# Optimization experiments

Measured on AMD Instinct MI355X. Metric: run time of the kernel, lower is better.

## Reference

```python
import jax, jax.numpy as jnp
import numpy as np

B, T, C, H = 4, 2048, 768, 64

def setup_inputs() -> dict:
    key = jax.random.key(0)
    kx, kq, kk, kv = jax.random.split(key, 4)
    x = jax.random.normal(kx, (B, T, C), dtype=jnp.float32)
    # torch Linear(C->H, bias=False): y = x @ W with W [C, H]
    s = 1.0 / np.sqrt(C)
    Wq = jax.random.normal(kq, (C, H), dtype=jnp.float32) * s
    Wk = jax.random.normal(kk, (C, H), dtype=jnp.float32) * s
    Wv = jax.random.normal(kv, (C, H), dtype=jnp.float32) * s
    return {"x": x, "Wq": Wq, "Wk": Wk, "Wv": Wv}

def reference(x, Wq, Wk, Wv):
    Bx, Tx, Cx = x.shape
    q = jnp.einsum('btc,ch->bth', x, Wq)
    k = jnp.einsum('btc,ch->bth', x, Wk)
    v = jnp.einsum('btc,ch->bth', x, Wv)
    # NOTE: original scales by C**-0.5 (n_embeddings), not head_size**-0.5
    w = jnp.einsum('bqh,bkh->bqk', q, k) * (Cx ** -0.5)  # [B, T, T]
    causal = jnp.tril(jnp.ones((Tx, Tx), dtype=bool))
    w = jnp.where(causal, w, -jnp.inf)
    w = jax.nn.softmax(w, axis=-1)
    # dropout: eval mode (identity)
    out = jnp.einsum('bqk,bkh->bqh', w, v)  # [B, T, H]
    return out
```

## Files before the change

kernel.cpp:

```cpp
#include <hip/hip_runtime.h>
#include <math.h>

#define TB 2048
#define CB 768
#define NB 4
#define NROWS (NB * TB)
#define NSMAX 32
#define WGPB 528

typedef __attribute__((ext_vector_type(8))) short bf16x8;
typedef __attribute__((ext_vector_type(4))) float f32x4;
typedef __attribute__((ext_vector_type(2))) float f32x2;
typedef __attribute__((ext_vector_type(2))) unsigned int u32x2;
typedef __attribute__((ext_vector_type(4))) unsigned int u32x4;

__device__ inline unsigned short f2bf(float f) {
  union { float f; unsigned u; } v; v.f = f;
  unsigned r = v.u + 0x7FFFu + ((v.u >> 16) & 1u);
  return (unsigned short)(r >> 16);
}
__device__ inline unsigned pack2bf(float a, float b) {
  return (unsigned)f2bf(a) | ((unsigned)f2bf(b) << 16);
}
__device__ inline float bf2f(unsigned short u) {
  union { unsigned u; float f; } v; v.u = (unsigned)u << 16; return v.f;
}

__global__ void cvt_w_kernel(const float* __restrict__ Wq, const float* __restrict__ Wk,
                             const float* __restrict__ Wv, unsigned short* __restrict__ Wt) {
  __shared__ float tw[64][65];
  const float* W = (blockIdx.y == 0) ? Wq : (blockIdx.y == 1) ? Wk : Wv;
  const int c0 = blockIdx.x * 64;
  const int row = threadIdx.x >> 2, seg = threadIdx.x & 3;
#pragma unroll
  for (int i = 0; i < 4; ++i) {
    float4 f = *(const float4*)(W + (size_t)(c0 + row) * 64 + seg * 16 + i * 4);
    tw[row][seg * 16 + i * 4 + 0] = f.x;
    tw[row][seg * 16 + i * 4 + 1] = f.y;
    tw[row][seg * 16 + i * 4 + 2] = f.z;
    tw[row][seg * 16 + i * 4 + 3] = f.w;
  }
  __syncthreads();
  const int j = threadIdx.x >> 2, cq = threadIdx.x & 3;
  unsigned short* dst = Wt + (size_t)(blockIdx.y * 64 + j) * CB + c0 + cq * 16;
  u32x4 ua, ub;
#pragma unroll
  for (int i = 0; i < 4; ++i) ua[i] = pack2bf(tw[cq * 16 + 2 * i][j], tw[cq * 16 + 2 * i + 1][j]);
#pragma unroll
  for (int i = 0; i < 4; ++i) ub[i] = pack2bf(tw[cq * 16 + 8 + 2 * i][j], tw[cq * 16 + 9 + 2 * i][j]);
  *(u32x4*)dst = ua;
  *(u32x4*)(dst + 8) = ub;
}

__launch_bounds__(256)
__global__ void proj_direct_kernel(const float* __restrict__ x,
                                   const unsigned short* __restrict__ Wt,
                                   unsigned short* __restrict__ q,
                                   unsigned short* __restrict__ k,
                                   unsigned short* __restrict__ vT) {
  __shared__ __align__(16) unsigned short xs[16 * 64];
  __shared__ float tr[64][17];
  const int tid = threadIdx.x;
  const int wv = tid >> 6;
  const int l = tid & 63;
  const int lrow = l & 15, lg = l >> 4;
  const int m0 = blockIdx.x * 16;
  const int srow = tid >> 4;
  const int sq = tid & 15;
  const float* xp = x + (size_t)(m0 + srow) * CB + sq * 4;
  const int swz = (srow & 7) << 4;

  f32x4 acc[3];
#pragma unroll
  for (int n = 0; n < 3; ++n) acc[n] = (f32x4){0.f, 0.f, 0.f, 0.f};

  float4 f = *(const float4*)xp;
  for (int k0 = 0; k0 < CB; k0 += 64) {
    {
      u32x2 c;
      c.x = pack2bf(f.x, f.y);
      c.y = pack2bf(f.z, f.w);
      *(u32x2*)((char*)xs + srow * 128 + ((sq * 8) ^ swz)) = c;
    }
    if (k0 + 64 < CB) f = *(const float4*)(xp + k0 + 64);
    __syncthreads();

#pragma unroll
    for (int s = 0; s < 2; ++s) {
      bf16x8 af = *(const bf16x8*)((const char*)xs + lrow * 128 +
                                   ((s * 64 + lg * 16) ^ ((lrow & 7) << 4)));
#pragma unroll
      for (int nf = 0; nf < 3; ++nf) {
        int col = wv * 48 + nf * 16 + lrow;
        bf16x8 bfr = *(const bf16x8*)(Wt + (size_t)col * CB + k0 + s * 32 + lg * 8);
        acc[nf] = __builtin_amdgcn_mfma_f32_16x16x32_bf16(af, bfr, acc[nf], 0, 0, 0);
      }
    }
    __syncthreads();
  }

#pragma unroll
  for (int nf = 0; nf < 3; ++nf) {
    int j = wv * 48 + nf * 16 + lrow;
#pragma unroll
    for (int r = 0; r < 4; ++r) {
      int grow = m0 + lg * 4 + r;
      if (j < 64)       q[(size_t)grow * 64 + j] = f2bf(acc[nf][r]);
      else if (j < 128) k[(size_t)grow * 64 + (j - 64)] = f2bf(acc[nf][r]);
      else              tr[j - 128][lg * 4 + r] = acc[nf][r];
    }
  }
  __syncthreads();
  {
    const int b = m0 >> 11, t0 = m0 & (TB - 1);
    const int h = tid >> 2, tq = tid & 3;
    u32x2 pk;
    pk.x = pack2bf(tr[h][tq * 4 + 0], tr[h][tq * 4 + 1]);
    pk.y = pack2bf(tr[h][tq * 4 + 2], tr[h][tq * 4 + 3]);
    *(u32x2*)(vT + ((size_t)(b * 64 + h)) * TB + t0 + tq * 4) = pk;
  }
}

__launch_bounds__(256)
__global__ void attn_kernel(const unsigned short* __restrict__ q,
                            const unsigned short* __restrict__ k,
                            const unsigned short* __restrict__ vT,
                            unsigned short* __restrict__ PO, float* __restrict__ Mp,
                            float* __restrict__ Lp) {
  __shared__ __align__(16) char ksm[8192];
  __shared__ __align__(16) char vsm[8192];
  const int tid = threadIdx.x;
  const int wid = tid >> 6, l = tid & 63;
  const int lrow = l & 15, lg = l >> 4;
  const int b = blockIdx.y;
  const int w = blockIdx.x;

  int g = (int)((sqrtf((float)(8 * w + 1)) - 1.f) * 0.5f);
  while ((g + 1) * (g + 2) / 2 <= w) ++g;
  while (g * (g + 1) / 2 > w) --g;
  const int blk = w - g * (g + 1) / 2;
  const int kv0 = blk * 64;
  const bool last = (blk == g);
  const int qrow = (4 * g + wid) * 16 + lrow;

  const unsigned short* qb = q + (size_t)b * TB * 64;
  const char* kbb = (const char*)(k + (size_t)b * TB * 64);
  const unsigned short* vb = vT + (size_t)b * 64 * TB;

  const int srow = tid >> 2;
  const int sc = (tid & 3) * 32;
  float4 kg0 = *(const float4*)(kbb + (size_t)kv0 * 128 + tid * 32);
  float4 kg1 = *(const float4*)(kbb + (size_t)kv0 * 128 + tid * 32 + 16);
  const char* vrow = (const char*)(vb + (size_t)srow * TB + kv0);
  float4 vg0 = *(const float4*)(vrow + sc);
  float4 vg1 = *(const float4*)(vrow + sc + 16);

  bf16x8 qf[2];
#pragma unroll
  for (int s = 0; s < 2; ++s)
    qf[s] = *(const bf16x8*)(qb + (size_t)qrow * 64 + s * 32 + lg * 8);

  {
    const int kswz_w = (srow & 7) << 4;
    *(float4*)(ksm + srow * 128 + ((sc + 0) ^ kswz_w)) = kg0;
    *(float4*)(ksm + srow * 128 + ((sc + 16) ^ kswz_w)) = kg1;
    const int vswz_w = (srow & 3) << 5;
    *(float4*)(vsm + srow * 128 + ((sc + 0) ^ vswz_w)) = vg0;
    *(float4*)(vsm + srow * 128 + ((sc + 16) ^ vswz_w)) = vg1;
  }
  __syncthreads();

  const int kswz = (lrow & 7) << 4;
  f32x4 S[4];
#pragma unroll
  for (int cf = 0; cf < 4; ++cf) S[cf] = (f32x4){0.f, 0.f, 0.f, 0.f};
#pragma unroll
  for (int cf = 0; cf < 4; ++cf) {
    const char* kp = ksm + (cf * 16 + lrow) * 128;
#pragma unroll
    for (int s = 0; s < 2; ++s) {
      bf16x8 kf = *(const bf16x8*)(kp + ((s * 64 + lg * 16) ^ kswz));
      S[cf] = __builtin_amdgcn_mfma_f32_16x16x32_bf16(kf, qf[s], S[cf], 0, 0, 0);
    }
  }

  const float scale = 0.03608439182435161f;
  float tmx = -INFINITY;
#pragma unroll
  for (int cf = 0; cf < 4; ++cf)
#pragma unroll
    for (int r = 0; r < 4; ++r) {
      float vv = S[cf][r] * scale;
      if (last) {
        int kvi = kv0 + cf * 16 + lg * 4 + r;
        vv = (kvi > qrow) ? -INFINITY : vv;
      }
      S[cf][r] = vv;
      tmx = fmaxf(tmx, vv);
    }
  tmx = fmaxf(tmx, __shfl_xor(tmx, 16));
  tmx = fmaxf(tmx, __shfl_xor(tmx, 32));

  float lsl = 0.f;
  float p[4][4];
#pragma unroll
  for (int cf = 0; cf < 4; ++cf)
#pragma unroll
    for (int r = 0; r < 4; ++r) {
      float pe = __expf(S[cf][r] - tmx);
      p[cf][r] = pe;
      lsl += pe;
    }
  union { unsigned u[4]; bf16x8 v; } pbu[2];
#pragma unroll
  for (int s = 0; s < 2; ++s) {
    pbu[s].u[0] = pack2bf(p[2 * s][0], p[2 * s][1]);
    pbu[s].u[1] = pack2bf(p[2 * s][2], p[2 * s][3]);
    pbu[s].u[2] = pack2bf(p[2 * s + 1][0], p[2 * s + 1][1]);
    pbu[s].u[3] = pack2bf(p[2 * s + 1][2], p[2 * s + 1][3]);
  }

  f32x4 o[4];
#pragma unroll
  for (int hf = 0; hf < 4; ++hf) o[hf] = (f32x4){0.f, 0.f, 0.f, 0.f};
  const int rswz = (lrow & 3) << 5;
#pragma unroll
  for (int s = 0; s < 2; ++s)
#pragma unroll
    for (int hf = 0; hf < 4; ++hf) {
      int r = hf * 16 + lrow;
      int a1 = r * 128 + ((s * 64 + lg * 8) ^ rswz);
      u32x2 lo = *(const u32x2*)(vsm + a1);
      u32x2 hi = *(const u32x2*)(vsm + (a1 ^ 32));
      union { unsigned u[4]; bf16x8 v; } vfu;
      vfu.u[0] = lo.x; vfu.u[1] = lo.y; vfu.u[2] = hi.x; vfu.u[3] = hi.y;
      o[hf] = __builtin_amdgcn_mfma_f32_16x16x32_bf16(vfu.v, pbu[s].v, o[hf], 0, 0, 0);
    }

  float ls = lsl;
  ls += __shfl_xor(ls, 16);
  ls += __shfl_xor(ls, 32);

  size_t rowg = (size_t)blk * NROWS + b * TB + qrow;
  unsigned short* pop = PO + rowg * 64 + lg * 4;
#pragma unroll
  for (int hf = 0; hf < 4; ++hf) {
    u32x2 pk;
    pk.x = pack2bf(o[hf][0], o[hf][1]);
    pk.y = pack2bf(o[hf][2], o[hf][3]);
    *(u32x2*)(pop + hf * 16) = pk;
  }
  if (lg == 0) {
    Mp[rowg] = tmx;
    Lp[rowg] = ls;
  }
}

__global__ void attn_reduce_kernel(const unsigned short* __restrict__ PO,
                                   const float* __restrict__ Mp,
                                   const float* __restrict__ Lp,
                                   float* __restrict__ out) {
  int id = blockIdx.x * 256 + threadIdx.x;
  if (id >= NROWS * 32) return;
  int row = id >> 5, h0 = (id & 31) * 2;
  int t = row & (TB - 1);
  int ns = (t >> 6) + 1;
  float M = -INFINITY;
#pragma unroll 4
  for (int s = 0; s < ns; ++s) M = fmaxf(M, Mp[(size_t)s * NROWS + row]);
  float L = 0.f, a0 = 0.f, a1 = 0.f;
#pragma unroll 4
  for (int s = 0; s < ns; ++s) {
    float w = __expf(Mp[(size_t)s * NROWS + row] - M);
    L += Lp[(size_t)s * NROWS + row] * w;
    unsigned pv = *(const unsigned*)(PO + ((size_t)s * NROWS + row) * 64 + h0);
    a0 += bf2f((unsigned short)(pv & 0xffff)) * w;
    a1 += bf2f((unsigned short)(pv >> 16)) * w;
  }
  float rL = 1.f / L;
  f32x2 r; r.x = a0 * rL; r.y = a1 * rL;
  *(f32x2*)(out + (size_t)row * 64 + h0) = r;
}

extern "C" void kernel_launch(void* const* d_in, const int* in_sizes, int n_in,
                              void* d_out, int out_size, void* d_ws, size_t ws_size,
                              hipStream_t stream) {
  const float* x  = (const float*)d_in[0];
  const float* Wq = (const float*)d_in[1];
  const float* Wk = (const float*)d_in[2];
  const float* Wv = (const float*)d_in[3];
  float* out = (float*)d_out;

  unsigned short* Wt = (unsigned short*)d_ws;
  unsigned short* qb = Wt + 192 * CB;
  unsigned short* kb = qb + (size_t)NROWS * 64;
  unsigned short* vT = kb + (size_t)NROWS * 64;
  char* scratch = (char*)(vT + (size_t)NROWS * 64);

  unsigned short* PO = (unsigned short*)scratch;
  float* Mp = (float*)(scratch + (size_t)NSMAX * NROWS * 64 * 2);
  float* Lp = Mp + (size_t)NSMAX * NROWS;

  hipLaunchKernelGGL(cvt_w_kernel, dim3(12, 3), dim3(256), 0, stream,
                     Wq, Wk, Wv, Wt);
  hipLaunchKernelGGL(proj_direct_kernel, dim3(NROWS / 16), dim3(256), 0, stream,
                     x, Wt, qb, kb, vT);
  hipLaunchKernelGGL(attn_kernel, dim3(WGPB, NB), dim3(256), 0, stream,
                     qb, kb, vT, PO, Mp, Lp);
  hipLaunchKernelGGL(attn_reduce_kernel, dim3((NROWS * 32) / 256), dim3(256), 0, stream,
                     PO, Mp, Lp, out);
}
```

Baseline: 56.76 us.

## Process two 64-key blocks per attention workgroup to halve split partials

Each attention workgroup now loads two consecutive 64-wide K/V blocks (128 keys) into double LDS buffers and computes a joint softmax over both before writing one partial. The number of split partials per query row drops from up to 32 to up to 16, which halves partial-output writes and the reduce kernel's loop and memory traffic. The price is fewer, larger workgroups with more LDS per block, which lowers parallelism and occupancy. The group-index decoding is rewritten for the new per-group block counts.

New measurement: 51.07 us. 10.0% less time.

```diff
diff --git a/kernel.cpp b/kernel.cpp
--- a/kernel.cpp
+++ b/kernel.cpp
@@ -5,8 +5,8 @@
 #define CB 768
 #define NB 4
 #define NROWS (NB * TB)
-#define NSMAX 32
-#define WGPB 528
+#define NSMAX 16
+#define WGPB 272
 
 typedef __attribute__((ext_vector_type(8))) short bf16x8;
 typedef __attribute__((ext_vector_type(4))) float f32x4;
@@ -24,6 +24,10 @@
 }
 __device__ inline float bf2f(unsigned short u) {
   union { unsigned u; float f; } v; v.u = (unsigned)u << 16; return v.f;
+}
+__device__ inline int groupP(int g) {
+  int m = g >> 1;
+  return (g & 1) ? (m + 1) * (m + 1) : m * (m + 1);
 }
 
 __global__ void cvt_w_kernel(const float* __restrict__ Wq, const float* __restrict__ Wk,
@@ -127,20 +131,22 @@
                             const unsigned short* __restrict__ vT,
                             unsigned short* __restrict__ PO, float* __restrict__ Mp,
                             float* __restrict__ Lp) {
-  __shared__ __align__(16) char ksm[8192];
-  __shared__ __align__(16) char vsm[8192];
+  __shared__ __align__(16) char ksm[2][8192];
+  __shared__ __align__(16) char vsm[2][8192];
   const int tid = threadIdx.x;
   const int wid = tid >> 6, l = tid & 63;
   const int lrow = l & 15, lg = l >> 4;
   const int b = blockIdx.y;
   const int w = blockIdx.x;
 
-  int g = (int)((sqrtf((float)(8 * w + 1)) - 1.f) * 0.5f);
-  while ((g + 1) * (g + 2) / 2 <= w) ++g;
-  while (g * (g + 1) / 2 > w) --g;
-  const int blk = w - g * (g + 1) / 2;
-  const int kv0 = blk * 64;
-  const bool last = (blk == g);
+  int g = (int)(2.f * sqrtf((float)w));
+  if (g > 31) g = 31;
+  while (g < 31 && groupP(g + 1) <= w) ++g;
+  while (g > 0 && groupP(g) > w) --g;
+  const int b128 = w - groupP(g);
+  const int s64a = 2 * b128, s64b = 2 * b128 + 1;
+  const bool has1 = (s64b <= g);
+  const int kv0a = s64a * 64, kv0b = s64b * 64;
   const int qrow = (4 * g + wid) * 16 + lrow;
 
   const unsigned short* qb = q + (size_t)b * TB * 64;
@@ -149,99 +155,173 @@
 
   const int srow = tid >> 2;
   const int sc = (tid & 3) * 32;
-  float4 kg0 = *(const float4*)(kbb + (size_t)kv0 * 128 + tid * 32);
-  float4 kg1 = *(const float4*)(kbb + (size_t)kv0 * 128 + tid * 32 + 16);
-  const char* vrow = (const char*)(vb + (size_t)srow * TB + kv0);
-  float4 vg0 = *(const float4*)(vrow + sc);
-  float4 vg1 = *(const float4*)(vrow + sc + 16);
+  const int kswz_w = (srow & 7) << 4;
+  const int vswz_w = (srow & 3) << 5;
+
+  float4 ka0 = *(const float4*)(kbb + (size_t)kv0a * 128 + tid * 32);
+  float4 ka1 = *(const float4*)(kbb + (size_t)kv0a * 128 + tid * 32 + 16);
+  const char* vrowa = (const char*)(vb + (size_t)srow * TB + kv0a);
+  float4 va0 = *(const float4*)(vrowa + sc);
+  float4 va1 = *(const float4*)(vrowa + sc + 16);
 
   bf16x8 qf[2];
 #pragma unroll
   for (int s = 0; s < 2; ++s)
     qf[s] = *(const bf16x8*)(qb + (size_t)qrow * 64 + s * 32 + lg * 8);
 
-  {
-    const int kswz_w = (srow & 7) << 4;
-    *(float4*)(ksm + srow * 128 + ((sc + 0) ^ kswz_w)) = kg0;
-    *(float4*)(ksm + srow * 128 + ((sc + 16) ^ kswz_w)) = kg1;
-    const int vswz_w = (srow & 3) << 5;
-    *(float4*)(vsm + srow * 128 + ((sc + 0) ^ vswz_w)) = vg0;
-    *(float4*)(vsm + srow * 128 + ((sc + 16) ^ vswz_w)) = vg1;
+  *(float4*)(ksm[0] + srow * 128 + ((sc + 0) ^ kswz_w)) = ka0;
+  *(float4*)(ksm[0] + srow * 128 + ((sc + 16) ^ kswz_w)) = ka1;
+  *(float4*)(vsm[0] + srow * 128 + ((sc + 0) ^ vswz_w)) = va0;
+  *(float4*)(vsm[0] + srow * 128 + ((sc + 16) ^ vswz_w)) = va1;
+
+  if (has1) {
+    float4 kb0 = *(const float4*)(kbb + (size_t)kv0b * 128 + tid * 32);
+    float4 kb1 = *(const float4*)(kbb + (size_t)kv0b * 128 + tid * 32 + 16);
+    const char* vrowb = (const char*)(vb + (size_t)srow * TB + kv0b);
+    float4 vb0 = *(const float4*)(vrowb + sc);
+    float4 vb1 = *(const float4*)(vrowb + sc + 16);
+    *(float4*)(ksm[1] + srow * 128 + ((sc + 0) ^ kswz_w)) = kb0;
+    *(float4*)(ksm[1] + srow * 128 + ((sc + 16) ^ kswz_w)) = kb1;
+    *(float4*)(vsm[1] + srow * 128 + ((sc + 0) ^ vswz_w)) = vb0;
+    *(float4*)(vsm[1] + srow * 128 + ((sc + 16) ^ vswz_w)) = vb1;
   }
   __syncthreads();
 
   const int kswz = (lrow & 7) << 4;
-  f32x4 S[4];
-#pragma unroll
-  for (int cf = 0; cf < 4; ++cf) S[cf] = (f32x4){0.f, 0.f, 0.f, 0.f};
+  const float scale = 0.03608439182435161f;
+
+  f32x4 S0[4];
+#pragma unroll
+  for (int cf = 0; cf < 4; ++cf) S0[cf] = (f32x4){0.f, 0.f, 0.f, 0.f};
 #pragma unroll
   for (int cf = 0; cf < 4; ++cf) {
-    const char* kp = ksm + (cf * 16 + lrow) * 128;
+    const char* kp = ksm[0] + (cf * 16 + lrow) * 128;
 #pragma unroll
     for (int s = 0; s < 2; ++s) {
       bf16x8 kf = *(const bf16x8*)(kp + ((s * 64 + lg * 16) ^ kswz));
-      S[cf] = __builtin_amdgcn_mfma_f32_16x16x32_bf16(kf, qf[s], S[cf], 0, 0, 0);
-    }
-  }
-
-  const float scale = 0.03608439182435161f;
+      S0[cf] = __builtin_amdgcn_mfma_f32_16x16x32_bf16(kf, qf[s], S0[cf], 0, 0, 0);
+    }
+  }
   float tmx = -INFINITY;
-#pragma unroll
-  for (int cf = 0; cf < 4; ++cf)
-#pragma unroll
-    for (int r = 0; r < 4; ++r) {
-      float vv = S[cf][r] * scale;
-      if (last) {
-        int kvi = kv0 + cf * 16 + lg * 4 + r;
-        vv = (kvi > qrow) ? -INFINITY : vv;
-      }
-      S[cf][r] = vv;
-      tmx = fmaxf(tmx, vv);
-    }
+  {
+    const bool msk = (s64a == g);
+#pragma unroll
+    for (int cf = 0; cf < 4; ++cf)
+#pragma unroll
+      for (int r = 0; r < 4; ++r) {
+        float vv = S0[cf][r] * scale;
+        if (msk) {
+          int kvi = kv0a + cf * 16 + lg * 4 + r;
+          vv = (kvi > qrow) ? -INFINITY : vv;
+        }
+        S0[cf][r] = vv;
+        tmx = fmaxf(tmx, vv);
+      }
+  }
+  f32x4 S1[4];
+  if (has1) {
+#pragma unroll
+    for (int cf = 0; cf < 4; ++cf) S1[cf] = (f32x4){0.f, 0.f, 0.f, 0.f};
+#pragma unroll
+    for (int cf = 0; cf < 4; ++cf) {
+      const char* kp = ksm[1] + (cf * 16 + lrow) * 128;
+#pragma unroll
+      for (int s = 0; s < 2; ++s) {
+        bf16x8 kf = *(const bf16x8*)(kp + ((s * 64 + lg * 16) ^ kswz));
+        S1[cf] = __builtin_amdgcn_mfma_f32_16x16x32_bf16(kf, qf[s], S1[cf], 0, 0, 0);
+      }
+    }
+    const bool msk = (s64b == g);
+#pragma unroll
+    for (int cf = 0; cf < 4; ++cf)
+#pragma unroll
+      for (int r = 0; r < 4; ++r) {
+        float vv = S1[cf][r] * scale;
+        if (msk) {
+          int kvi = kv0b + cf * 16 + lg * 4 + r;
+          vv = (kvi > qrow) ? -INFINITY : vv;
+        }
+        S1[cf][r] = vv;
+        tmx = fmaxf(tmx, vv);
+      }
+  }
   tmx = fmaxf(tmx, __shfl_xor(tmx, 16));
   tmx = fmaxf(tmx, __shfl_xor(tmx, 32));
 
   float lsl = 0.f;
-  float p[4][4];
-#pragma unroll
-  for (int cf = 0; cf < 4; ++cf)
-#pragma unroll
-    for (int r = 0; r < 4; ++r) {
-      float pe = __expf(S[cf][r] - tmx);
-      p[cf][r] = pe;
-      lsl += pe;
-    }
-  union { unsigned u[4]; bf16x8 v; } pbu[2];
-#pragma unroll
-  for (int s = 0; s < 2; ++s) {
-    pbu[s].u[0] = pack2bf(p[2 * s][0], p[2 * s][1]);
-    pbu[s].u[1] = pack2bf(p[2 * s][2], p[2 * s][3]);
-    pbu[s].u[2] = pack2bf(p[2 * s + 1][0], p[2 * s + 1][1]);
-    pbu[s].u[3] = pack2bf(p[2 * s + 1][2], p[2 * s + 1][3]);
-  }
-
   f32x4 o[4];
 #pragma unroll
   for (int hf = 0; hf < 4; ++hf) o[hf] = (f32x4){0.f, 0.f, 0.f, 0.f};
   const int rswz = (lrow & 3) << 5;
-#pragma unroll
-  for (int s = 0; s < 2; ++s)
-#pragma unroll
-    for (int hf = 0; hf < 4; ++hf) {
-      int r = hf * 16 + lrow;
-      int a1 = r * 128 + ((s * 64 + lg * 8) ^ rswz);
-      u32x2 lo = *(const u32x2*)(vsm + a1);
-      u32x2 hi = *(const u32x2*)(vsm + (a1 ^ 32));
-      union { unsigned u[4]; bf16x8 v; } vfu;
-      vfu.u[0] = lo.x; vfu.u[1] = lo.y; vfu.u[2] = hi.x; vfu.u[3] = hi.y;
-      o[hf] = __builtin_amdgcn_mfma_f32_16x16x32_bf16(vfu.v, pbu[s].v, o[hf], 0, 0, 0);
-    }
+
+  {
+    float p[4][4];
+#pragma unroll
+    for (int cf = 0; cf < 4; ++cf)
+#pragma unroll
+      for (int r = 0; r < 4; ++r) {
+        float pe = __expf(S0[cf][r] - tmx);
+        p[cf][r] = pe;
+        lsl += pe;
+      }
+    union { unsigned u[4]; bf16x8 v; } pbu[2];
+#pragma unroll
+    for (int s = 0; s < 2; ++s) {
+      pbu[s].u[0] = pack2bf(p[2 * s][0], p[2 * s][1]);
+      pbu[s].u[1] = pack2bf(p[2 * s][2], p[2 * s][3]);
+      pbu[s].u[2] = pack2bf(p[2 * s + 1][0], p[2 * s + 1][1]);
+      pbu[s].u[3] = pack2bf(p[2 * s + 1][2], p[2 * s + 1][3]);
+    }
+#pragma unroll
+    for (int s = 0; s < 2; ++s)
+#pragma unroll
+      for (int hf = 0; hf < 4; ++hf) {
+        int r = hf * 16 + lrow;
+        int a1 = r * 128 + ((s * 64 + lg * 8) ^ rswz);
+        u32x2 lo = *(const u32x2*)(vsm[0] + a1);
+        u32x2 hi = *(const u32x2*)(vsm[0] + (a1 ^ 32));
+        union { unsigned u[4]; bf16x8 v; } vfu;
+        vfu.u[0] = lo.x; vfu.u[1] = lo.y; vfu.u[2] = hi.x; vfu.u[3] = hi.y;
+        o[hf] = __builtin_amdgcn_mfma_f32_16x16x32_bf16(vfu.v, pbu[s].v, o[hf], 0, 0, 0);
+      }
+  }
+  if (has1) {
+    float p[4][4];
+#pragma unroll
+    for (int cf = 0; cf < 4; ++cf)
+#pragma unroll
+      for (int r = 0; r < 4; ++r) {
+        float pe = __expf(S1[cf][r] - tmx);
+        p[cf][r] = pe;
+        lsl += pe;
+      }
+    union { unsigned u[4]; bf16x8 v; } pbu[2];
+#pragma unroll
+    for (int s = 0; s < 2; ++s) {
+      pbu[s].u[0] = pack2bf(p[2 * s][0], p[2 * s][1]);
+      pbu[s].u[1] = pack2bf(p[2 * s][2], p[2 * s][3]);
+      pbu[s].u[2] = pack2bf(p[2 * s + 1][0], p[2 * s + 1][1]);
+      pbu[s].u[3] = pack2bf(p[2 * s + 1][2], p[2 * s + 1][3]);
+    }
+#pragma unroll
+    for (int s = 0; s < 2; ++s)
+#pragma unroll
+      for (int hf = 0; hf < 4; ++hf) {
+        int r = hf * 16 + lrow;
+        int a1 = r * 128 + ((s * 64 + lg * 8) ^ rswz);
+        u32x2 lo = *(const u32x2*)(vsm[1] + a1);
+        u32x2 hi = *(const u32x2*)(vsm[1] + (a1 ^ 32));
+        union { unsigned u[4]; bf16x8 v; } vfu;
+        vfu.u[0] = lo.x; vfu.u[1] = lo.y; vfu.u[2] = hi.x; vfu.u[3] = hi.y;
+        o[hf] = __builtin_amdgcn_mfma_f32_16x16x32_bf16(vfu.v, pbu[s].v, o[hf], 0, 0, 0);
+      }
+  }
 
   float ls = lsl;
   ls += __shfl_xor(ls, 16);
   ls += __shfl_xor(ls, 32);
 
-  size_t rowg = (size_t)blk * NROWS + b * TB + qrow;
+  size_t rowg = (size_t)b128 * NROWS + b * TB + qrow;
   unsigned short* pop = PO + rowg * 64 + lg * 4;
 #pragma unroll
   for (int hf = 0; hf < 4; ++hf) {
@@ -264,7 +344,7 @@
   if (id >= NROWS * 32) return;
   int row = id >> 5, h0 = (id & 31) * 2;
   int t = row & (TB - 1);
-  int ns = (t >> 6) + 1;
+  int ns = (t >> 7) + 1;
   float M = -INFINITY;
 #pragma unroll 4
   for (int s = 0; s < ns; ++s) M = fmaxf(M, Mp[(size_t)s * NROWS + row]);
```
